# Kernel optimization log

Hardware: AMD Instinct MI355X
Metric: run time of the kernel (lower is better)

Reference implementation:

```python
import jax, jax.numpy as jnp
import numpy as np

INPUT_DIM = 512
OUTPUT_DIM = 512
DEGREE = 7
ALPHA = 0.5


def setup_inputs() -> dict:
    key = jax.random.key(0)
    kx, kc = jax.random.split(key)
    x = jax.random.normal(kx, (8192, INPUT_DIM), dtype=jnp.float32)
    std = 1.0 / (INPUT_DIM * (DEGREE + 1))
    laguerre_coeffs = jax.random.normal(kc, (INPUT_DIM, OUTPUT_DIM, DEGREE + 1), dtype=jnp.float32) * std
    return {"x": x, "laguerre_coeffs": laguerre_coeffs}


def reference(x, laguerre_coeffs):
    # x: [B, I] -> tanh squashed
    xt = jnp.tanh(x.reshape(-1, INPUT_DIM))
    # Build Laguerre basis L_0..L_degree via the standard recurrence:
    # k*L_k = (2(k-1)+1+alpha - x)*L_{k-1} - (k-1+alpha)*L_{k-2}
    L0 = jnp.ones_like(xt)
    basis = [L0]
    if DEGREE > 0:
        L1 = 1.0 + ALPHA - xt
        basis.append(L1)
        Lkm2, Lkm1 = L0, L1
        for k in range(2, DEGREE + 1):
            Lk = ((2 * (k - 1) + 1 + ALPHA - xt) * Lkm1 - (k - 1 + ALPHA) * Lkm2) / k
            basis.append(Lk)
            Lkm2, Lkm1 = Lkm1, Lk
    laguerre = jnp.stack(basis, axis=-1)  # [B, I, D+1]
    y = jnp.einsum('bid,iod->bo', laguerre, laguerre_coeffs)
    return y
```

## Files before the change

kernel.cpp:

```cpp
#include <hip/hip_runtime.h>

#define B_ROWS 8192
#define IN_DIM 512
#define OUT_DIM 512
#define NDEG 8
#define KDIM (IN_DIM * NDEG)
#define ZSLICES 4
#define NKT 16

typedef short bf16x8 __attribute__((ext_vector_type(8)));
typedef float f32x4  __attribute__((ext_vector_type(4)));

__device__ __forceinline__ unsigned short f2bf(float f) {
  unsigned u = __float_as_uint(f);
  u += 0x7fffu + ((u >> 16) & 1u);
  return (unsigned short)(u >> 16);
}

__device__ __forceinline__ void laguerre8(float t, float* L) {
  L[0] = 1.0f;
  L[1] = 1.5f - t;
#pragma unroll
  for (int k = 2; k < NDEG; ++k)
    L[k] = ((2.0f * (float)k - 0.5f - t) * L[k - 1] -
            ((float)k - 0.5f) * L[k - 2]) * (1.0f / (float)k);
}

__device__ __forceinline__ float ftanh(float x) {
  float e2 = __expf(2.0f * x);
  return (e2 - 1.0f) * (1.0f / (e2 + 1.0f));
}

__device__ __forceinline__ uint4 bpack(float xv) {
  float L[NDEG];
  laguerre8(ftanh(xv), L);
  uint4 v;
  v.x = (unsigned)f2bf(L[0]) | ((unsigned)f2bf(L[1]) << 16);
  v.y = (unsigned)f2bf(L[2]) | ((unsigned)f2bf(L[3]) << 16);
  v.z = (unsigned)f2bf(L[4]) | ((unsigned)f2bf(L[5]) << 16);
  v.w = (unsigned)f2bf(L[6]) | ((unsigned)f2bf(L[7]) << 16);
  return v;
}


__global__ void prep_kernel(const float* __restrict__ x, const float* __restrict__ cf,
                            unsigned short* __restrict__ A, unsigned short* __restrict__ Bt) {
  int g = blockIdx.x;
  if (g < (B_ROWS * IN_DIM) / 256) {
    int idx = g * 256 + threadIdx.x;
    int b = idx >> 9, i = idx & 511;
    uint4 v = bpack(x[idx]);
    int h = b >> 7, rb = b & 127, t = i >> 3, c = i & 7;
    size_t chunk = ((size_t)(h * 64 + t)) * 1024 + (rb >> 6) * 512 + (rb & 63) * 8 + (c ^ (rb & 7));
    ((uint4*)A)[chunk] = v;
  } else {
    int idx = (g - (B_ROWS * IN_DIM) / 256) * 256 + threadIdx.x;
    int i = idx >> 9, o = idx & 511;
    const float4* cp = (const float4*)(cf + (size_t)idx * 8);
    float4 c0 = cp[0], c1 = cp[1];
    uint4 v;
    v.x = (unsigned)f2bf(c0.x) | ((unsigned)f2bf(c0.y) << 16);
    v.y = (unsigned)f2bf(c0.z) | ((unsigned)f2bf(c0.w) << 16);
    v.z = (unsigned)f2bf(c1.x) | ((unsigned)f2bf(c1.y) << 16);
    v.w = (unsigned)f2bf(c1.z) | ((unsigned)f2bf(c1.w) << 16);
    int h = o >> 7, rb = o & 127, t = i >> 3, c = i & 7;
    size_t chunk = ((size_t)(h * 64 + t)) * 1024 + (rb >> 6) * 512 + (rb & 63) * 8 + (c ^ (rb & 7));
    ((uint4*)Bt)[chunk] = v;
  }
}


#define PH(buf, mq, ks, LOADBF, VMW, ...)                                          \
  {                                                                                \
    const unsigned short* Ab_ = lds + (buf)*16384 + wm*8192 + (mq)*4096 + arow*64; \
    _Pragma("unroll") for (int m4 = 0; m4 < 4; ++m4)                               \
      af[m4] = *(const bf16x8*)(Ab_ + m4*1024 + (e ^ ((ks)*32)));                  \
    if (LOADBF) {                                                                  \
      const unsigned short* Bb_ = lds + 32768 + (buf)*16384 + (wn>>1)*8192         \
                                  + (wn&1)*4096 + arow*64;                         \
      _Pragma("unroll") for (int ni = 0; ni < 4; ++ni)                             \
        bfr[ni] = *(const bf16x8*)(Bb_ + ni*1024 + (e ^ ((ks)*32)));               \
    }                                                                              \
    __builtin_amdgcn_s_barrier();             \
    __VA_ARGS__;                             \
    asm volatile("s_waitcnt lgkmcnt(0)" ::: "memory");                             \
    __builtin_amdgcn_sched_barrier(0);                                             \
    __builtin_amdgcn_s_setprio(1);                                                 \
    _Pragma("unroll") for (int m4 = 0; m4 < 4; ++m4)                               \
      _Pragma("unroll") for (int ni = 0; ni < 4; ++ni)                             \
        acc[(mq)*4+m4][ni] = __builtin_amdgcn_mfma_f32_16x16x32_bf16(              \
            af[m4], bfr[ni], acc[(mq)*4+m4][ni], 0, 0, 0);                         \
    __builtin_amdgcn_s_setprio(0);                                                 \
    if ((VMW) == 1) { asm volatile("s_waitcnt vmcnt(2)" ::: "memory");             \
                      __builtin_amdgcn_sched_barrier(0);                           \
                      __builtin_amdgcn_s_barrier(); }        \
    if ((VMW) == 2) { asm volatile("s_waitcnt vmcnt(0)" ::: "memory");             \
                      __builtin_amdgcn_sched_barrier(0);                           \
                      __builtin_amdgcn_s_barrier(); }                              \
  }

__global__ __launch_bounds__(512, 2) void gemm_kernel(const unsigned short* __restrict__ A,
                                                      const unsigned short* __restrict__ Bt,
                                                      unsigned short* __restrict__ P) {
  __shared__ unsigned short lds[65536];

  const int tid = threadIdx.x;
  const int lane = tid & 63;
  const int w = tid >> 6;
  const int wm = w >> 2, wn = w & 3;

  const int g = blockIdx.x;
  const int j0 = g >> 3, xx = g & 7;
  const int My = ((j0 >> 3) << 3) | xx;
  const int n = (j0 >> 2) & 1;
  const int z = j0 & 3;

  const uint4* Ag = (const uint4*)A;
  const uint4* Bg = (const uint4*)Bt;

  const int arow = lane & 15, hi = lane >> 4;
  const int e = (hi ^ (arow & 7)) * 8;

  f32x4 zero = {0.f, 0.f, 0.f, 0.f};
  f32x4 acc[8][4];
#pragma unroll
  for (int mi = 0; mi < 8; ++mi)
#pragma unroll
    for (int ni = 0; ni < 4; ++ni) acc[mi][ni] = zero;

  auto STAGE_H = [&](int isB, int h, int tile, int buf) {
    const uint4* src = isB ? Bg : Ag;
    const int rowblk = (isB ? n * 2 : My * 2) + h;
    const size_t c0 = ((size_t)(rowblk * 64 + z * NKT + tile)) * 1024 + w * 64 + lane;
    unsigned short* d = lds + isB * 32768 + buf * 16384 + h * 8192 + w * 512;
    __builtin_amdgcn_global_load_lds(
        (const __attribute__((address_space(1))) unsigned int*)(src + c0),
        (__attribute__((address_space(3))) unsigned int*)d, 16, 0, 0);
    __builtin_amdgcn_global_load_lds(
        (const __attribute__((address_space(1))) unsigned int*)(src + c0 + 512),
        (__attribute__((address_space(3))) unsigned int*)(d + 4096), 16, 0, 0);
  };

  bf16x8 af[4], bfr[4];

  STAGE_H(0, 0, 0, 0); STAGE_H(0, 1, 0, 0);
  STAGE_H(1, 0, 0, 0); STAGE_H(1, 1, 0, 0);
  STAGE_H(1, 0, 1, 1);
  asm volatile("s_waitcnt vmcnt(2)" ::: "memory");
  __builtin_amdgcn_sched_barrier(0);
  __builtin_amdgcn_s_barrier();

  for (int it = 0; it < 7; ++it) {
    const int t1 = 2 * it + 1, t2 = 2 * it + 2, t3 = 2 * it + 3;
    PH(0, 0, 0, 1, 0, STAGE_H(1, 1, t1, 1));
    PH(0, 1, 0, 0, 0, STAGE_H(0, 0, t1, 1));
    PH(0, 0, 1, 1, 0, STAGE_H(0, 1, t1, 1));
    PH(0, 1, 1, 0, 1, STAGE_H(1, 0, t2, 0));
    PH(1, 0, 0, 1, 0, STAGE_H(0, 0, t2, 0));
    PH(1, 1, 0, 0, 0, STAGE_H(0, 1, t2, 0));
    PH(1, 0, 1, 1, 0, STAGE_H(1, 1, t2, 0));
    PH(1, 1, 1, 0, 1, STAGE_H(1, 0, t3, 1));
  }
  PH(0, 0, 0, 1, 0, STAGE_H(1, 1, 15, 1));
  PH(0, 1, 0, 0, 0, STAGE_H(0, 0, 15, 1));
  PH(0, 0, 1, 1, 0, STAGE_H(0, 1, 15, 1));
  PH(0, 1, 1, 0, 2, (void)0);
  PH(1, 0, 0, 1, 0, (void)0);
  PH(1, 1, 0, 0, 0, (void)0);
  PH(1, 0, 1, 1, 0, (void)0);
  PH(1, 1, 1, 0, 0, (void)0);
  __syncthreads();

  unsigned short* W = lds + w * 8192;
#pragma unroll
  for (int mi = 0; mi < 8; ++mi)
#pragma unroll
    for (int ni = 0; ni < 4; ++ni) {
      int col = ni * 16 + arow;
      int c8 = col >> 3, cpos = col & 7;
#pragma unroll
      for (int r = 0; r < 4; ++r) {
        int row = mi * 16 + hi * 4 + r;
        W[row * 64 + ((c8 ^ (row & 7)) << 3) + cpos] = f2bf(acc[mi][ni][r]);
      }
    }
  const int rr = lane >> 3, cc = lane & 7;
#pragma unroll
  for (int it = 0; it < 16; ++it) {
    int row = it * 8 + rr;
    uint4 v = *(uint4*)&W[row * 64 + ((cc ^ (row & 7)) << 3)];
    size_t pr = ((size_t)z * B_ROWS + My * 256 + wm * 128 + row) * 512 + n * 256 + wn * 64 + cc * 8;
    *(uint4*)&P[pr] = v;
  }
}

__global__ void reduce_kernel(const unsigned short* __restrict__ P, float* __restrict__ out) {
  size_t t = (size_t)blockIdx.x * 256 + threadIdx.x;
  const uint4* p = (const uint4*)P;
  const size_t stride = (size_t)B_ROWS * OUT_DIM / 8;
  float s[8] = {0, 0, 0, 0, 0, 0, 0, 0};
#pragma unroll
  for (int zz = 0; zz < ZSLICES; ++zz) {
    uint4 v = p[t + zz * stride];
    unsigned q[4] = {v.x, v.y, v.z, v.w};
#pragma unroll
    for (int j = 0; j < 4; ++j) {
      s[2 * j]     += __uint_as_float((q[j] & 0xffffu) << 16);
      s[2 * j + 1] += __uint_as_float(q[j] & 0xffff0000u);
    }
  }
  float4 o0 = {s[0], s[1], s[2], s[3]}, o1 = {s[4], s[5], s[6], s[7]};
  ((float4*)out)[t * 2]     = o0;
  ((float4*)out)[t * 2 + 1] = o1;
}

__global__ void naive_kernel(const float* __restrict__ x, const float* __restrict__ c,
                             float* __restrict__ out) {
  __shared__ float bas[IN_DIM * NDEG];
  int b = blockIdx.x;
  for (int i = threadIdx.x; i < IN_DIM; i += 256) {
    float t = tanhf(x[(size_t)b * IN_DIM + i]);
    float L[NDEG];
    laguerre8(t, L);
#pragma unroll
    for (int d = 0; d < NDEG; ++d) bas[i * NDEG + d] = L[d];
  }
  __syncthreads();
  for (int o = threadIdx.x; o < OUT_DIM; o += 256) {
    float acc = 0.f;
    for (int i = 0; i < IN_DIM; ++i) {
      const float* cp = c + ((size_t)i * OUT_DIM + o) * NDEG;
#pragma unroll
      for (int d = 0; d < NDEG; ++d) acc += bas[i * NDEG + d] * cp[d];
    }
    out[(size_t)b * OUT_DIM + o] = acc;
  }
}

extern "C" void kernel_launch(void* const* d_in, const int* in_sizes, int n_in,
                              void* d_out, int out_size, void* d_ws, size_t ws_size,
                              hipStream_t stream) {
  const float* x    = (const float*)d_in[0];
  const float* coef = (const float*)d_in[1];
  float* out = (float*)d_out;

  const size_t A_B  = (size_t)B_ROWS * KDIM * 2;
  const size_t P_B  = (size_t)ZSLICES * B_ROWS * OUT_DIM * 2;
  const size_t BT_B = (size_t)OUT_DIM * KDIM * 2;

  if (ws_size >= A_B + P_B + BT_B) {
    unsigned short* Abuf = (unsigned short*)d_ws;
    unsigned short* Pp   = (unsigned short*)((char*)d_ws + A_B);
    unsigned short* Bt   = (unsigned short*)((char*)d_ws + A_B + P_B);
    prep_kernel<<<(B_ROWS * IN_DIM) / 256 + (IN_DIM * OUT_DIM) / 256, 256, 0, stream>>>(x, coef, Abuf, Bt);
    gemm_kernel<<<256, 512, 0, stream>>>(Abuf, Bt, Pp);
    reduce_kernel<<<(B_ROWS * OUT_DIM / 8) / 256, 256, 0, stream>>>(Pp, out);
  } else {
    naive_kernel<<<B_ROWS, 256, 0, stream>>>(x, coef, out);
  }
}
```

Baseline: 66.66 us.

## Double-buffer MFMA register fragments to overlap LDS reads with matrix math

Replaces the per-phase load-then-compute macro with split LDS-read and MFMA macros that use two sets of A/B register fragments. Each phase now issues the next fragment's LDS reads before running MFMAs on the current fragment, so LDS latency is hidden behind matrix work. It also drops most of the per-phase s_barriers and explicit lgkmcnt waits, keeping only the barriers around buffer swaps. The cost is higher VGPR pressure, which could cause spills or lower occupancy at two blocks per CU. Without explicit lgkmcnt waits, the code relies on the compiler to insert correct waits.

```diff
diff --git a/kernel.cpp b/kernel.cpp
--- a/kernel.cpp
+++ b/kernel.cpp
@@ -70,34 +70,26 @@
 }
 
 
-#define PH(buf, mq, ks, LOADBF, VMW, ...)                                          \
-  {                                                                                \
-    const unsigned short* Ab_ = lds + (buf)*16384 + wm*8192 + (mq)*4096 + arow*64; \
+#define SB __builtin_amdgcn_sched_barrier(0)
+
+#define LDA(SET, buf, mq, ks)                                                      \
+  { const unsigned short* Ab_ = lds + (buf)*16384 + wm*8192 + (mq)*4096 + arow*64; \
     _Pragma("unroll") for (int m4 = 0; m4 < 4; ++m4)                               \
-      af[m4] = *(const bf16x8*)(Ab_ + m4*1024 + (e ^ ((ks)*32)));                  \
-    if (LOADBF) {                                                                  \
-      const unsigned short* Bb_ = lds + 32768 + (buf)*16384 + (wn>>1)*8192         \
-                                  + (wn&1)*4096 + arow*64;                         \
-      _Pragma("unroll") for (int ni = 0; ni < 4; ++ni)                             \
-        bfr[ni] = *(const bf16x8*)(Bb_ + ni*1024 + (e ^ ((ks)*32)));               \
-    }                                                                              \
-    __builtin_amdgcn_s_barrier();             \
-    __VA_ARGS__;                             \
-    asm volatile("s_waitcnt lgkmcnt(0)" ::: "memory");                             \
-    __builtin_amdgcn_sched_barrier(0);                                             \
-    __builtin_amdgcn_s_setprio(1);                                                 \
+      SET[m4] = *(const bf16x8*)(Ab_ + m4*1024 + (e ^ ((ks)*32))); }
+
+#define LDB_(SET, buf, ks)                                                         \
+  { const unsigned short* Bb_ = lds + 32768 + (buf)*16384 + (wn>>1)*8192           \
+                                + (wn&1)*4096 + arow*64;                           \
+    _Pragma("unroll") for (int ni = 0; ni < 4; ++ni)                               \
+      SET[ni] = *(const bf16x8*)(Bb_ + ni*1024 + (e ^ ((ks)*32))); }
+
+#define MM(ASET, BSET, mq)                                                         \
+  { __builtin_amdgcn_s_setprio(1);                                                 \
     _Pragma("unroll") for (int m4 = 0; m4 < 4; ++m4)                               \
       _Pragma("unroll") for (int ni = 0; ni < 4; ++ni)                             \
         acc[(mq)*4+m4][ni] = __builtin_amdgcn_mfma_f32_16x16x32_bf16(              \
-            af[m4], bfr[ni], acc[(mq)*4+m4][ni], 0, 0, 0);                         \
-    __builtin_amdgcn_s_setprio(0);                                                 \
-    if ((VMW) == 1) { asm volatile("s_waitcnt vmcnt(2)" ::: "memory");             \
-                      __builtin_amdgcn_sched_barrier(0);                           \
-                      __builtin_amdgcn_s_barrier(); }        \
-    if ((VMW) == 2) { asm volatile("s_waitcnt vmcnt(0)" ::: "memory");             \
-                      __builtin_amdgcn_sched_barrier(0);                           \
-                      __builtin_amdgcn_s_barrier(); }                              \
-  }
+            ASET[m4], BSET[ni], acc[(mq)*4+m4][ni], 0, 0, 0);                      \
+    __builtin_amdgcn_s_setprio(0); }
 
 __global__ __launch_bounds__(512, 2) void gemm_kernel(const unsigned short* __restrict__ A,
                                                       const unsigned short* __restrict__ Bt,
@@ -141,34 +133,49 @@
         (__attribute__((address_space(3))) unsigned int*)(d + 4096), 16, 0, 0);
   };
 
-  bf16x8 af[4], bfr[4];
+  bf16x8 afA[4], afB[4], bfA[4], bfB[4];
 
   STAGE_H(0, 0, 0, 0); STAGE_H(0, 1, 0, 0);
   STAGE_H(1, 0, 0, 0); STAGE_H(1, 1, 0, 0);
   STAGE_H(1, 0, 1, 1);
   asm volatile("s_waitcnt vmcnt(2)" ::: "memory");
-  __builtin_amdgcn_sched_barrier(0);
+  SB;
   __builtin_amdgcn_s_barrier();
+  SB;
+  LDA(afA, 0, 0, 0); LDB_(bfA, 0, 0);
 
   for (int it = 0; it < 7; ++it) {
     const int t1 = 2 * it + 1, t2 = 2 * it + 2, t3 = 2 * it + 3;
-    PH(0, 0, 0, 1, 0, STAGE_H(1, 1, t1, 1));
-    PH(0, 1, 0, 0, 0, STAGE_H(0, 0, t1, 1));
-    PH(0, 0, 1, 1, 0, STAGE_H(0, 1, t1, 1));
-    PH(0, 1, 1, 0, 1, STAGE_H(1, 0, t2, 0));
-    PH(1, 0, 0, 1, 0, STAGE_H(0, 0, t2, 0));
-    PH(1, 1, 0, 0, 0, STAGE_H(0, 1, t2, 0));
-    PH(1, 0, 1, 1, 0, STAGE_H(1, 1, t2, 0));
-    PH(1, 1, 1, 0, 1, STAGE_H(1, 0, t3, 1));
-  }
-  PH(0, 0, 0, 1, 0, STAGE_H(1, 1, 15, 1));
-  PH(0, 1, 0, 0, 0, STAGE_H(0, 0, 15, 1));
-  PH(0, 0, 1, 1, 0, STAGE_H(0, 1, 15, 1));
-  PH(0, 1, 1, 0, 2, (void)0);
-  PH(1, 0, 0, 1, 0, (void)0);
-  PH(1, 1, 0, 0, 0, (void)0);
-  PH(1, 0, 1, 1, 0, (void)0);
-  PH(1, 1, 1, 0, 0, (void)0);
+    LDA(afB, 0, 1, 0); STAGE_H(1, 1, t1, 1); SB; MM(afA, bfA, 0);
+    LDA(afA, 0, 0, 1); LDB_(bfB, 0, 1); STAGE_H(0, 0, t1, 1); SB; MM(afB, bfA, 1);
+    LDA(afB, 0, 1, 1); STAGE_H(0, 1, t1, 1); SB; MM(afA, bfB, 0);
+    __builtin_amdgcn_s_barrier(); SB;
+    STAGE_H(1, 0, t2, 0); SB;
+    MM(afB, bfB, 1);
+    asm volatile("s_waitcnt vmcnt(2)" ::: "memory"); SB;
+    __builtin_amdgcn_s_barrier(); SB;
+    LDA(afA, 1, 0, 0); LDB_(bfA, 1, 0);
+    LDA(afB, 1, 1, 0); STAGE_H(0, 0, t2, 0); SB; MM(afA, bfA, 0);
+    LDA(afA, 1, 0, 1); LDB_(bfB, 1, 1); STAGE_H(0, 1, t2, 0); SB; MM(afB, bfA, 1);
+    LDA(afB, 1, 1, 1); STAGE_H(1, 1, t2, 0); SB; MM(afA, bfB, 0);
+    __builtin_amdgcn_s_barrier(); SB;
+    STAGE_H(1, 0, t3, 1); SB;
+    MM(afB, bfB, 1);
+    asm volatile("s_waitcnt vmcnt(2)" ::: "memory"); SB;
+    __builtin_amdgcn_s_barrier(); SB;
+    LDA(afA, 0, 0, 0); LDB_(bfA, 0, 0);
+  }
+  LDA(afB, 0, 1, 0); STAGE_H(1, 1, 15, 1); SB; MM(afA, bfA, 0);
+  LDA(afA, 0, 0, 1); LDB_(bfB, 0, 1); STAGE_H(0, 0, 15, 1); SB; MM(afB, bfA, 1);
+  LDA(afB, 0, 1, 1); STAGE_H(0, 1, 15, 1); SB; MM(afA, bfB, 0);
+  MM(afB, bfB, 1);
+  asm volatile("s_waitcnt vmcnt(0)" ::: "memory"); SB;
+  __builtin_amdgcn_s_barrier(); SB;
+  LDA(afA, 1, 0, 0); LDB_(bfA, 1, 0);
+  LDA(afB, 1, 1, 0); SB; MM(afA, bfA, 0);
+  LDA(afA, 1, 0, 1); LDB_(bfB, 1, 1); SB; MM(afB, bfA, 1);
+  LDA(afB, 1, 1, 1); SB; MM(afA, bfB, 0);
+  MM(afB, bfB, 1);
   __syncthreads();
 
   unsigned short* W = lds + w * 8192;
```

After: 66.15 us. No clear change (-0.8%).
